# Kernel optimization log

Hardware: AMD Instinct MI355X
Metric: run time of the kernel (lower is better)

The kernel has to match this reference:

```python
import jax, jax.numpy as jnp
import numpy as np

# Static config (matches init_kwargs)
DIM = 1024
INTER = 512
E = 8          # n_routed_experts
TOP_K = 2      # n_activated_experts
ROUTE_SCALE = 1.0


def setup_inputs() -> dict:
    key = jax.random.key(0)
    ks = jax.random.split(key, 8)
    s_d = 1.0 / np.sqrt(DIM)
    s_f = 1.0 / np.sqrt(INTER)
    x = jax.random.normal(ks[0], (2, 2048, DIM), dtype=jnp.float32)
    gate_w = jax.random.uniform(ks[1], (E, DIM), jnp.float32, -s_d, s_d)
    # routed expert weights, stacked: gate/up are [E, F, D], down is [E, D, F]
    wg = jax.random.uniform(ks[2], (E, INTER, DIM), jnp.float32, -s_d, s_d)
    wu = jax.random.uniform(ks[3], (E, INTER, DIM), jnp.float32, -s_d, s_d)
    wd = jax.random.uniform(ks[4], (E, DIM, INTER), jnp.float32, -s_f, s_f)
    # shared expert (n_shared_experts = 1)
    sg = jax.random.uniform(ks[5], (INTER, DIM), jnp.float32, -s_d, s_d)
    su = jax.random.uniform(ks[6], (INTER, DIM), jnp.float32, -s_d, s_d)
    sd = jax.random.uniform(ks[7], (DIM, INTER), jnp.float32, -s_f, s_f)
    return {"x": x, "gate_w": gate_w, "wg": wg, "wu": wu, "wd": wd,
            "sg": sg, "su": su, "sd": sd}


def reference(x, gate_w, wg, wu, wd, sg, su, sd):
    B, S, D = x.shape
    xf = x.reshape(-1, D)                       # [N, D]
    N = xf.shape[0]

    # ---- Gate (eval mode: no expert_bias, softmax scoring, 1 group) ----
    scores = jax.nn.softmax(xf @ gate_w.T, axis=-1)          # [N, E]
    _, idx = jax.lax.top_k(scores, TOP_K)                    # [N, K]
    weights = jnp.take_along_axis(scores, idx, axis=-1) * ROUTE_SCALE  # [N, K]

    # Combine weights as dense [N, E] (scatter-add of top-k weights) --
    # equivalent to the sort/dispatch + weighted scatter_add combine.
    cw = jnp.zeros((N, E), dtype=xf.dtype)
    cw = cw.at[jnp.arange(N)[:, None], idx].add(weights)     # [N, E]

    # ---- Routed experts: SwiGLU per expert ----
    g = jnp.einsum('nd,efd->nef', xf, wg)                    # [N, E, F]
    u = jnp.einsum('nd,efd->nef', xf, wu)                    # [N, E, F]
    h = jax.nn.silu(g) * u                                   # [N, E, F]
    y = jnp.einsum('nef,edf->ned', h, wd)                    # [N, E, D]
    routed = jnp.einsum('ned,ne->nd', y, cw)                 # [N, D]

    # ---- Shared expert (always active) ----
    shared = (jax.nn.silu(xf @ sg.T) * (xf @ su.T)) @ sd.T   # [N, D]

    return (routed + shared).reshape(B, S, D)
```

## Files before the change

### kernel.cpp

```cpp
#include <hip/hip_runtime.h>
#include <hip/hip_bf16.h>

constexpr int NTOK = 4096;
constexpr int DIMD = 1024;
constexpr int FINT = 512;
constexpr int NEXP = 8;

typedef __attribute__((ext_vector_type(8))) short bf16x8;
typedef __attribute__((ext_vector_type(4))) float f32x4;
typedef __attribute__((ext_vector_type(8))) unsigned short u16x8;

__device__ __forceinline__ f32x4 mfma16(bf16x8 a, bf16x8 b, f32x4 c) {
  return __builtin_amdgcn_mfma_f32_16x16x32_bf16(a, b, c, 0, 0, 0);
}

__device__ __forceinline__ void gload16(const void* g, void* l) {
  __builtin_amdgcn_global_load_lds(
      (const __attribute__((address_space(1))) void*)g,
      (__attribute__((address_space(3))) void*)l, 16, 0, 0);
}

__device__ __forceinline__ unsigned short f2bf(float f) {
  unsigned u = __float_as_uint(f);
  u += 0x7fffu + ((u >> 16) & 1u);
  return (unsigned short)(u >> 16);
}

__global__ __launch_bounds__(256) void cast_all(
    const float* __restrict__ x,  const float* __restrict__ wg,
    const float* __restrict__ wu, const float* __restrict__ wd,
    const float* __restrict__ sg, const float* __restrict__ su,
    const float* __restrict__ sd,
    unsigned short* __restrict__ xb,  unsigned short* __restrict__ w1b,
    unsigned short* __restrict__ wdb, unsigned short* __restrict__ s1b,
    unsigned short* __restrict__ sdb) {
  const int seg = blockIdx.y;
  const int i = blockIdx.x * 256 + threadIdx.x;
  const float* src; unsigned short* dst;
  size_t si = (size_t)i * 8, di;
  int n8;
  if (seg == 0) {
    n8 = NTOK * DIMD / 8; if (i >= n8) return;
    src = x; dst = xb; di = si;
  } else if (seg == 1 || seg == 2) {
    n8 = NEXP * FINT * DIMD / 8; if (i >= n8) return;
    int e = (int)(si >> 19), f = (int)((si >> 10) & 511), d = (int)(si & 1023);
    int r = ((f >> 4) << 5) + (seg == 2 ? 16 : 0) + (f & 15);
    src = (seg == 1) ? wg : wu; dst = w1b;
    di = (((size_t)e << 10) + r) * 1024 + d;
  } else if (seg == 3) {
    n8 = NEXP * DIMD * FINT / 8; if (i >= n8) return;
    src = wd; dst = wdb; di = si;
  } else if (seg == 4 || seg == 5) {
    n8 = FINT * DIMD / 8; if (i >= n8) return;
    int f = (int)((si >> 10) & 511), d = (int)(si & 1023);
    int r = ((f >> 4) << 5) + (seg == 5 ? 16 : 0) + (f & 15);
    src = (seg == 4) ? sg : su; dst = s1b;
    di = (size_t)r * 1024 + d;
  } else {
    n8 = DIMD * FINT / 8; if (i >= n8) return;
    src = sd; dst = sdb; di = si;
  }
  const float4* s4 = (const float4*)(src + si);
  float4 a = s4[0], b = s4[1];
  u16x8 o;
  o[0] = f2bf(a.x); o[1] = f2bf(a.y); o[2] = f2bf(a.z); o[3] = f2bf(a.w);
  o[4] = f2bf(b.x); o[5] = f2bf(b.y); o[6] = f2bf(b.z); o[7] = f2bf(b.w);
  *(u16x8*)(dst + di) = o;
}

__global__ __launch_bounds__(256) void gate_logits(const float* __restrict__ x,
                                                   const float* __restrict__ gw,
                                                   int* __restrict__ eid,
                                                   float2* __restrict__ w12) {
  const int wid = threadIdx.x >> 6;
  const int lane = threadIdx.x & 63;
  const int n = blockIdx.x * 4 + wid;

  const float4* xr = (const float4*)(x + (size_t)n * DIMD);
  float4 xv[4];
#pragma unroll
  for (int j = 0; j < 4; ++j) xv[j] = xr[lane + 64 * j];

  double acc[NEXP];
#pragma unroll
  for (int e = 0; e < NEXP; ++e) {
    const float4* g = (const float4*)(gw + (size_t)e * DIMD);
    double a = 0.0;
#pragma unroll
    for (int j = 0; j < 4; ++j) {
      float4 gv = g[lane + 64 * j];
      a += (double)xv[j].x * (double)gv.x + (double)xv[j].y * (double)gv.y
         + (double)xv[j].z * (double)gv.z + (double)xv[j].w * (double)gv.w;
    }
    acc[e] = a;
  }
#pragma unroll
  for (int e = 0; e < NEXP; ++e) {
#pragma unroll
    for (int off = 32; off > 0; off >>= 1) acc[e] += __shfl_xor(acc[e], off);
  }

  if (lane == 0) {
    float logit[NEXP];
#pragma unroll
    for (int e = 0; e < NEXP; ++e) logit[e] = (float)acc[e];
    int i1 = 0; float v1 = logit[0];
#pragma unroll
    for (int e = 1; e < NEXP; ++e) if (logit[e] > v1) { v1 = logit[e]; i1 = e; }
    int i2 = -1; float v2 = -1e30f;
#pragma unroll
    for (int e = 0; e < NEXP; ++e) if (e != i1 && logit[e] > v2) { v2 = logit[e]; i2 = e; }
    float s = 0.f;
#pragma unroll
    for (int e = 0; e < NEXP; ++e) s += expf(logit[e] - v1);
    float w1 = 1.f / s;
    float w2 = expf(v2 - v1) / s;
    eid[n] = i1 | (i2 << 4);
    w12[n] = make_float2(w1, w2);
  }
}

__global__ __launch_bounds__(1024) void dispatch_scan(const int* __restrict__ eid,
                                                      const float2* __restrict__ w12,
                                                      int* __restrict__ cnt,
                                                      int* __restrict__ rowTok,
                                                      float* __restrict__ rowW,
                                                      int2* __restrict__ gslot) {
  const int th = threadIdx.x;
  const int lane = th & 63;
  const int wv = th >> 6;

  int e0[4], e1[4];
  float2 wp[4];
  unsigned long long c0 = 0, c1 = 0;
#pragma unroll
  for (int j = 0; j < 4; ++j) {
    int n = th * 4 + j;
    int p = eid[n];
    wp[j] = w12[n];
    int a = p & 15, b = (p >> 4) & 15;
    e0[j] = a; e1[j] = b;
    unsigned long long ia = 1ull << (16 * (a & 3));
    if (a < 4) c0 += ia; else c1 += ia;
    unsigned long long ib = 1ull << (16 * (b & 3));
    if (b < 4) c0 += ib; else c1 += ib;
  }

  unsigned long long s0 = c0, s1 = c1;
#pragma unroll
  for (int off = 1; off < 64; off <<= 1) {
    unsigned long long u0 = __shfl_up(s0, off);
    unsigned long long u1 = __shfl_up(s1, off);
    if (lane >= off) { s0 += u0; s1 += u1; }
  }

  __shared__ unsigned long long wt0[16], wt1[16];
  __shared__ int ebaseS[NEXP];
  if (lane == 63) { wt0[wv] = s0; wt1[wv] = s1; }
  __syncthreads();

  unsigned long long b0 = 0, b1 = 0;
  for (int w2 = 0; w2 < 16; ++w2)
    if (w2 < wv) { b0 += wt0[w2]; b1 += wt1[w2]; }

  if (th == 0) {
    unsigned long long t0 = 0, t1 = 0;
    for (int w2 = 0; w2 < 16; ++w2) { t0 += wt0[w2]; t1 += wt1[w2]; }
    int tot[NEXP];
#pragma unroll
    for (int e = 0; e < 4; ++e) {
      tot[e]     = (int)((t0 >> (16 * e)) & 0xffff);
      tot[e + 4] = (int)((t1 >> (16 * e)) & 0xffff);
    }
    int run = 0;
#pragma unroll
    for (int e = 0; e < NEXP; ++e) {
      cnt[e] = tot[e];
      cnt[8 + e] = run;
      ebaseS[e] = run;
      run += tot[e];
    }
  }

  unsigned long long x0 = b0 + s0 - c0;
  unsigned long long x1 = b1 + s1 - c1;

  __shared__ unsigned short posL[1024][8];
#pragma unroll
  for (int e = 0; e < 4; ++e) {
    posL[th][e]     = (unsigned short)((x0 >> (16 * e)) & 0xffff);
    posL[th][e + 4] = (unsigned short)((x1 >> (16 * e)) & 0xffff);
  }
  __syncthreads();

#pragma unroll
  for (int j = 0; j < 4; ++j) {
    int n = th * 4 + j;
    int a = e0[j];
    int pa = posL[th][a]; posL[th][a] = (unsigned short)(pa + 1);
    rowTok[a * NTOK + pa] = n; rowW[a * NTOK + pa] = wp[j].x;
    int b = e1[j];
    int pb = posL[th][b]; posL[th][b] = (unsigned short)(pb + 1);
    rowTok[b * NTOK + pb] = n; rowW[b * NTOK + pb] = wp[j].y;
    gslot[n] = make_int2(ebaseS[a] + pa, ebaseS[b] + pb);
  }
}


__global__ __launch_bounds__(512, 1) void gemm1_fused(
    const unsigned short* __restrict__ xb,
    const unsigned short* __restrict__ w1b,
    const unsigned short* __restrict__ s1b,
    unsigned short* __restrict__ hb,
    unsigned short* __restrict__ hs,
    const int* __restrict__ cnt,
    const int* __restrict__ rowTok,
    const unsigned short* __restrict__ zpg) {
  extern __shared__ unsigned char L[];
  const int e = blockIdx.x >> 2, ty = blockIdx.x & 3;
  const int tx = blockIdx.y;
  const bool RT = (e < NEXP);
  const int Te = RT ? cnt[e] : NTOK;
  const int m0 = tx * 256;
  if (m0 >= Te) return;
  const int n0 = ty * 256;

  const int t = threadIdx.x;
  const int w = t >> 6, lane = t & 63;
  const int wr = w >> 2, wc = w & 3;
  const int fr = lane & 15, hi = lane >> 4;
  const int koffl = ((hi ^ ((fr >> 1) & 3)) << 4);

  const unsigned short* w1e = RT ? w1b + (size_t)e * DIMD * DIMD : s1b;

  const unsigned short* apD[2];
  const unsigned short* bpD[2];
  int aoff[2], boff[2];
#pragma unroll
  for (int j = 0; j < 2; ++j) {
    int c = w * 128 + j * 64 + lane;
    int rowL = c >> 2;
    int seff = (c & 3) ^ ((c >> 3) & 3);
    int grow = m0 + rowL;
    const unsigned short* p;
    if (RT) p = (grow < Te) ? xb + (size_t)rowTok[e * NTOK + grow] * DIMD : zpg;
    else    p = xb + (size_t)grow * DIMD;
    apD[j] = p + seff * 8;
    bpD[j] = w1e + (size_t)(n0 + rowL) * DIMD + seff * 8;
    aoff[j] = c * 16;
    boff[j] = 65536 + c * 16;
  }

  f32x4 acc[8][4];
  f32x4 zero = {0.f, 0.f, 0.f, 0.f};
#pragma unroll
  for (int m = 0; m < 8; ++m)
#pragma unroll
    for (int n = 0; n < 4; ++n) acc[m][n] = zero;

  auto STAGE = [&](int buf, int tt, int q) {
    int slab = (buf * 2 + q) * 16384;
#pragma unroll
    for (int j = 0; j < 2; ++j) {
      gload16(apD[j] + tt * 64 + q * 32, L + slab + aoff[j]);
      gload16(bpD[j] + tt * 64 + q * 32, L + slab + boff[j]);
    }
  };
  auto COMPUTE = [&](int buf, int q) {
    int slab = (buf * 2 + q) * 16384;
    const unsigned char* LA = L + slab;
    const unsigned char* LB = L + 65536 + slab;
    bf16x8 Af[8], Bf[4];
#pragma unroll
    for (int m = 0; m < 8; ++m)
      Af[m] = *(const bf16x8*)(LA + (wr * 128 + m * 16 + fr) * 64 + koffl);
#pragma unroll
    for (int n = 0; n < 4; ++n)
      Bf[n] = *(const bf16x8*)(LB + (wc * 64 + n * 16 + fr) * 64 + koffl);
    __builtin_amdgcn_s_setprio(1);
#pragma unroll
    for (int n = 0; n < 4; ++n)
#pragma unroll
      for (int m = 0; m < 8; ++m) acc[m][n] = mfma16(Af[m], Bf[n], acc[m][n]);
    __builtin_amdgcn_s_setprio(0);
  };

  asm volatile("s_waitcnt vmcnt(0)" ::: "memory");
  __builtin_amdgcn_sched_barrier(0);
  STAGE(0, 0, 0);
  STAGE(0, 0, 1);

  constexpr int NT = DIMD / 64;
  for (int tt = 0; tt < NT; ++tt) {
    int buf = tt & 1;
#pragma unroll
    for (int q = 0; q < 2; ++q) {
      if (tt < NT - 1 || q == 0) asm volatile("s_waitcnt vmcnt(4)" ::: "memory");
      else                       asm volatile("s_waitcnt vmcnt(0)" ::: "memory");
      __builtin_amdgcn_sched_barrier(0);
      __builtin_amdgcn_s_barrier();
      __builtin_amdgcn_sched_barrier(0);
      if (tt + 1 < NT) STAGE(buf ^ 1, tt + 1, q);
      COMPUTE(buf, q);
    }
  }

  unsigned short* hbase = RT ? hb + (size_t)cnt[8 + e] * FINT : hs;
  const int fbase = ty * 128 + wc * 32 + fr;
#pragma unroll
  for (int m = 0; m < 8; ++m) {
#pragma unroll
    for (int r = 0; r < 4; ++r) {
      int row = m0 + wr * 128 + m * 16 + hi * 4 + r;
      if (row < Te) {
        float g0 = acc[m][0][r], u0 = acc[m][1][r];
        float g1 = acc[m][2][r], u1 = acc[m][3][r];
        hbase[(size_t)row * FINT + fbase]      = f2bf(g0 / (1.f + expf(-g0)) * u0);
        hbase[(size_t)row * FINT + fbase + 16] = f2bf(g1 / (1.f + expf(-g1)) * u1);
      }
    }
  }
}

__global__ __launch_bounds__(512, 1) void gemm2_fused(
    const unsigned short* __restrict__ hb,
    const unsigned short* __restrict__ hs,
    const unsigned short* __restrict__ wdb,
    const unsigned short* __restrict__ sdb,
    float* __restrict__ ybuf,
    float* __restrict__ out,
    const int* __restrict__ cnt,
    const float* __restrict__ rowW,
    const unsigned short* __restrict__ zpg) {
  extern __shared__ unsigned char L[];
  const int e = blockIdx.x >> 2, ty = blockIdx.x & 3;
  const int tx = blockIdx.y;
  const bool RT = (e < NEXP);
  const int Te = RT ? cnt[e] : NTOK;
  const int m0 = tx * 256;
  if (m0 >= Te) return;
  const int n0 = ty * 256;

  const int t = threadIdx.x;
  const int w = t >> 6, lane = t & 63;
  const int wr = w >> 2, wc = w & 3;
  const int fr = lane & 15, hi = lane >> 4;
  const int koffl = ((hi ^ ((fr >> 1) & 3)) << 4);

  const int gbase = RT ? cnt[8 + e] : 0;
  const unsigned short* he  = RT ? hb + (size_t)gbase * FINT : hs;
  const unsigned short* wde = RT ? wdb + (size_t)e * DIMD * FINT : sdb;

  const unsigned short* apD[2];
  const unsigned short* bpD[2];
  int aoff[2], boff[2];
#pragma unroll
  for (int j = 0; j < 2; ++j) {
    int c = w * 128 + j * 64 + lane;
    int rowL = c >> 2;
    int seff = (c & 3) ^ ((c >> 3) & 3);
    int grow = m0 + rowL;
    apD[j] = ((grow < Te) ? he + (size_t)grow * FINT : zpg) + seff * 8;
    bpD[j] = wde + (size_t)(n0 + rowL) * FINT + seff * 8;
    aoff[j] = c * 16;
    boff[j] = 65536 + c * 16;
  }

  f32x4 acc[8][4];
  f32x4 zero = {0.f, 0.f, 0.f, 0.f};
#pragma unroll
  for (int m = 0; m < 8; ++m)
#pragma unroll
    for (int n = 0; n < 4; ++n) acc[m][n] = zero;

  auto STAGE = [&](int buf, int tt, int q) {
    int slab = (buf * 2 + q) * 16384;
#pragma unroll
    for (int j = 0; j < 2; ++j) {
      gload16(apD[j] + tt * 64 + q * 32, L + slab + aoff[j]);
      gload16(bpD[j] + tt * 64 + q * 32, L + slab + boff[j]);
    }
  };
  auto COMPUTE = [&](int buf, int q) {
    int slab = (buf * 2 + q) * 16384;
    const unsigned char* LA = L + slab;
    const unsigned char* LB = L + 65536 + slab;
    bf16x8 Af[8], Bf[4];
#pragma unroll
    for (int m = 0; m < 8; ++m)
      Af[m] = *(const bf16x8*)(LA + (wr * 128 + m * 16 + fr) * 64 + koffl);
#pragma unroll
    for (int n = 0; n < 4; ++n)
      Bf[n] = *(const bf16x8*)(LB + (wc * 64 + n * 16 + fr) * 64 + koffl);
    __builtin_amdgcn_s_setprio(1);
#pragma unroll
    for (int n = 0; n < 4; ++n)
#pragma unroll
      for (int m = 0; m < 8; ++m) acc[m][n] = mfma16(Af[m], Bf[n], acc[m][n]);
    __builtin_amdgcn_s_setprio(0);
  };

  asm volatile("s_waitcnt vmcnt(0)" ::: "memory");
  __builtin_amdgcn_sched_barrier(0);
  STAGE(0, 0, 0);
  STAGE(0, 0, 1);

  constexpr int NT = FINT / 64;
  for (int tt = 0; tt < NT; ++tt) {
    int buf = tt & 1;
#pragma unroll
    for (int q = 0; q < 2; ++q) {
      if (tt < NT - 1 || q == 0) asm volatile("s_waitcnt vmcnt(4)" ::: "memory");
      else                       asm volatile("s_waitcnt vmcnt(0)" ::: "memory");
      __builtin_amdgcn_sched_barrier(0);
      __builtin_amdgcn_s_barrier();
      __builtin_amdgcn_sched_barrier(0);
      if (tt + 1 < NT) STAGE(buf ^ 1, tt + 1, q);
      COMPUTE(buf, q);
    }
  }

  const int colb = n0 + wc * 64;
#pragma unroll
  for (int m = 0; m < 8; ++m) {
#pragma unroll
    for (int r = 0; r < 4; ++r) {
      int row = m0 + wr * 128 + m * 16 + hi * 4 + r;
      if (row < Te) {
        if (RT) {
          float wt = rowW[e * NTOK + row];
          float* yr = ybuf + (size_t)(gbase + row) * DIMD;
#pragma unroll
          for (int n = 0; n < 4; ++n)
            yr[colb + n * 16 + fr] = wt * acc[m][n][r];
        } else {
          float* orow = out + (size_t)row * DIMD;
#pragma unroll
          for (int n = 0; n < 4; ++n)
            orow[colb + n * 16 + fr] = acc[m][n][r];
        }
      }
    }
  }
}

__global__ __launch_bounds__(256) void combine(const float* __restrict__ ybuf,
                                               const int2* __restrict__ gslot,
                                               float* __restrict__ out) {
  const int n = blockIdx.x;
  const int t = threadIdx.x;
  int2 gs = gslot[n];
  const float4* y1 = (const float4*)(ybuf + (size_t)gs.x * DIMD);
  const float4* y2 = (const float4*)(ybuf + (size_t)gs.y * DIMD);
  float4* o = (float4*)(out + (size_t)n * DIMD);
  float4 a = o[t], b = y1[t], c = y2[t];
  a.x += b.x + c.x; a.y += b.y + c.y; a.z += b.z + c.z; a.w += b.w + c.w;
  o[t] = a;
}

extern "C" void kernel_launch(void* const* d_in, const int* in_sizes, int n_in,
                              void* d_out, int out_size, void* d_ws, size_t ws_size,
                              hipStream_t stream) {
  const float* x  = (const float*)d_in[0];
  const float* gw = (const float*)d_in[1];
  const float* wg = (const float*)d_in[2];
  const float* wu = (const float*)d_in[3];
  const float* wd = (const float*)d_in[4];
  const float* sg = (const float*)d_in[5];
  const float* su = (const float*)d_in[6];
  const float* sd = (const float*)d_in[7];
  float* out = (float*)d_out;

  char* ws = (char*)d_ws;
  size_t off = 0;
  auto alloc = [&](size_t bytes) -> char* {
    char* p = ws + off;
    off += (bytes + 255) & ~(size_t)255;
    return p;
  };
  unsigned short* xb  = (unsigned short*)alloc((size_t)NTOK * DIMD * 2);
  unsigned short* w1b = (unsigned short*)alloc((size_t)NEXP * DIMD * DIMD * 2);
  unsigned short* wdb = (unsigned short*)alloc((size_t)NEXP * DIMD * FINT * 2);
  unsigned short* s1b = (unsigned short*)alloc((size_t)DIMD * DIMD * 2);
  unsigned short* sdb = (unsigned short*)alloc((size_t)DIMD * FINT * 2);
  unsigned short* hb  = (unsigned short*)alloc((size_t)2 * NTOK * FINT * 2);
  unsigned short* hs  = (unsigned short*)alloc((size_t)NTOK * FINT * 2);
  float*         ybuf = (float*)alloc((size_t)2 * NTOK * DIMD * 4);
  int*            cnt = (int*)alloc(256);
  int*         rowTok = (int*)alloc((size_t)NEXP * NTOK * 4);
  float*         rowW = (float*)alloc((size_t)NEXP * NTOK * 4);
  unsigned short* zpg = (unsigned short*)alloc((size_t)DIMD * 2);
  int*            eid = (int*)alloc((size_t)NTOK * 4);
  float2*         w12 = (float2*)alloc((size_t)NTOK * 8);
  int2*         gslot = (int2*)alloc((size_t)NTOK * 8);
  if (off > ws_size) return;

  hipFuncSetAttribute((const void*)gemm1_fused,
                      hipFuncAttributeMaxDynamicSharedMemorySize, 131072);
  hipFuncSetAttribute((const void*)gemm2_fused,
                      hipFuncAttributeMaxDynamicSharedMemorySize, 131072);

  hipMemsetAsync(zpg, 0, (size_t)DIMD * 2, stream);

  cast_all<<<dim3(2048, 7), 256, 0, stream>>>(x, wg, wu, wd, sg, su, sd,
                                              xb, w1b, wdb, s1b, sdb);

  gate_logits<<<NTOK / 4, 256, 0, stream>>>(x, gw, eid, w12);
  dispatch_scan<<<1, 1024, 0, stream>>>(eid, w12, cnt, rowTok, rowW, gslot);

  gemm1_fused<<<dim3(36, 16), 512, 131072, stream>>>(xb, w1b, s1b, hb, hs,
                                                     cnt, rowTok, zpg);
  gemm2_fused<<<dim3(36, 16), 512, 131072, stream>>>(hb, hs, wdb, sdb, ybuf, out,
                                                     cnt, rowW, zpg);
  combine<<<NTOK, 256, 0, stream>>>(ybuf, gslot, out);
}
```

Baseline: 114.5 us.

## Fold gate into cast kernel and restructure GEMM K-loop to one barrier pair per tile

```diff
diff --git a/kernel.cpp b/kernel.cpp
--- a/kernel.cpp
+++ b/kernel.cpp
@@ -30,11 +30,64 @@
     const float* __restrict__ x,  const float* __restrict__ wg,
     const float* __restrict__ wu, const float* __restrict__ wd,
     const float* __restrict__ sg, const float* __restrict__ su,
-    const float* __restrict__ sd,
+    const float* __restrict__ sd, const float* __restrict__ gw,
     unsigned short* __restrict__ xb,  unsigned short* __restrict__ w1b,
     unsigned short* __restrict__ wdb, unsigned short* __restrict__ s1b,
-    unsigned short* __restrict__ sdb) {
+    unsigned short* __restrict__ sdb,
+    int* __restrict__ eid, float2* __restrict__ w12) {
   const int seg = blockIdx.y;
+
+  if (seg == 7) {
+    if (blockIdx.x >= NTOK / 4) return;
+    const int wid = threadIdx.x >> 6;
+    const int lane = threadIdx.x & 63;
+    const int n = blockIdx.x * 4 + wid;
+
+    const float4* xr = (const float4*)(x + (size_t)n * DIMD);
+    float4 xv[4];
+#pragma unroll
+    for (int j = 0; j < 4; ++j) xv[j] = xr[lane + 64 * j];
+
+    double acc[NEXP];
+#pragma unroll
+    for (int e = 0; e < NEXP; ++e) {
+      const float4* g = (const float4*)(gw + (size_t)e * DIMD);
+      double a = 0.0;
+#pragma unroll
+      for (int j = 0; j < 4; ++j) {
+        float4 gv = g[lane + 64 * j];
+        a += (double)xv[j].x * (double)gv.x + (double)xv[j].y * (double)gv.y
+           + (double)xv[j].z * (double)gv.z + (double)xv[j].w * (double)gv.w;
+      }
+      acc[e] = a;
+    }
+#pragma unroll
+    for (int e = 0; e < NEXP; ++e) {
+#pragma unroll
+      for (int off = 32; off > 0; off >>= 1) acc[e] += __shfl_xor(acc[e], off);
+    }
+
+    if (lane == 0) {
+      float logit[NEXP];
+#pragma unroll
+      for (int e = 0; e < NEXP; ++e) logit[e] = (float)acc[e];
+      int i1 = 0; float v1 = logit[0];
+#pragma unroll
+      for (int e = 1; e < NEXP; ++e) if (logit[e] > v1) { v1 = logit[e]; i1 = e; }
+      int i2 = -1; float v2 = -1e30f;
+#pragma unroll
+      for (int e = 0; e < NEXP; ++e) if (e != i1 && logit[e] > v2) { v2 = logit[e]; i2 = e; }
+      float s = 0.f;
+#pragma unroll
+      for (int e = 0; e < NEXP; ++e) s += expf(logit[e] - v1);
+      float w1 = 1.f / s;
+      float w2 = expf(v2 - v1) / s;
+      eid[n] = i1 | (i2 << 4);
+      w12[n] = make_float2(w1, w2);
+    }
+    return;
+  }
+
   const int i = blockIdx.x * 256 + threadIdx.x;
   const float* src; unsigned short* dst;
   size_t si = (size_t)i * 8, di;
@@ -69,58 +122,6 @@
   *(u16x8*)(dst + di) = o;
 }
 
-__global__ __launch_bounds__(256) void gate_logits(const float* __restrict__ x,
-                                                   const float* __restrict__ gw,
-                                                   int* __restrict__ eid,
-                                                   float2* __restrict__ w12) {
-  const int wid = threadIdx.x >> 6;
-  const int lane = threadIdx.x & 63;
-  const int n = blockIdx.x * 4 + wid;
-
-  const float4* xr = (const float4*)(x + (size_t)n * DIMD);
-  float4 xv[4];
-#pragma unroll
-  for (int j = 0; j < 4; ++j) xv[j] = xr[lane + 64 * j];
-
-  double acc[NEXP];
-#pragma unroll
-  for (int e = 0; e < NEXP; ++e) {
-    const float4* g = (const float4*)(gw + (size_t)e * DIMD);
-    double a = 0.0;
-#pragma unroll
-    for (int j = 0; j < 4; ++j) {
-      float4 gv = g[lane + 64 * j];
-      a += (double)xv[j].x * (double)gv.x + (double)xv[j].y * (double)gv.y
-         + (double)xv[j].z * (double)gv.z + (double)xv[j].w * (double)gv.w;
-    }
-    acc[e] = a;
-  }
-#pragma unroll
-  for (int e = 0; e < NEXP; ++e) {
-#pragma unroll
-    for (int off = 32; off > 0; off >>= 1) acc[e] += __shfl_xor(acc[e], off);
-  }
-
-  if (lane == 0) {
-    float logit[NEXP];
-#pragma unroll
-    for (int e = 0; e < NEXP; ++e) logit[e] = (float)acc[e];
-    int i1 = 0; float v1 = logit[0];
-#pragma unroll
-    for (int e = 1; e < NEXP; ++e) if (logit[e] > v1) { v1 = logit[e]; i1 = e; }
-    int i2 = -1; float v2 = -1e30f;
-#pragma unroll
-    for (int e = 0; e < NEXP; ++e) if (e != i1 && logit[e] > v2) { v2 = logit[e]; i2 = e; }
-    float s = 0.f;
-#pragma unroll
-    for (int e = 0; e < NEXP; ++e) s += expf(logit[e] - v1);
-    float w1 = 1.f / s;
-    float w2 = expf(v2 - v1) / s;
-    eid[n] = i1 | (i2 << 4);
-    w12[n] = make_float2(w1, w2);
-  }
-}
-
 __global__ __launch_bounds__(1024) void dispatch_scan(const int* __restrict__ eid,
                                                       const float2* __restrict__ w12,
                                                       int* __restrict__ cnt,
@@ -267,43 +268,46 @@
       gload16(bpD[j] + tt * 64 + q * 32, L + slab + boff[j]);
     }
   };
-  auto COMPUTE = [&](int buf, int q) {
-    int slab = (buf * 2 + q) * 16384;
-    const unsigned char* LA = L + slab;
-    const unsigned char* LB = L + 65536 + slab;
-    bf16x8 Af[8], Bf[4];
-#pragma unroll
-    for (int m = 0; m < 8; ++m)
-      Af[m] = *(const bf16x8*)(LA + (wr * 128 + m * 16 + fr) * 64 + koffl);
-#pragma unroll
-    for (int n = 0; n < 4; ++n)
-      Bf[n] = *(const bf16x8*)(LB + (wc * 64 + n * 16 + fr) * 64 + koffl);
+  auto TILE = [&](int buf) {
+    bf16x8 Af[2][8], Bf[2][4];
+#pragma unroll
+    for (int q = 0; q < 2; ++q) {
+      int slab = (buf * 2 + q) * 16384;
+      const unsigned char* LA = L + slab;
+      const unsigned char* LB = L + 65536 + slab;
+#pragma unroll
+      for (int m = 0; m < 8; ++m)
+        Af[q][m] = *(const bf16x8*)(LA + (wr * 128 + m * 16 + fr) * 64 + koffl);
+#pragma unroll
+      for (int n = 0; n < 4; ++n)
+        Bf[q][n] = *(const bf16x8*)(LB + (wc * 64 + n * 16 + fr) * 64 + koffl);
+    }
     __builtin_amdgcn_s_setprio(1);
 #pragma unroll
-    for (int n = 0; n < 4; ++n)
-#pragma unroll
-      for (int m = 0; m < 8; ++m) acc[m][n] = mfma16(Af[m], Bf[n], acc[m][n]);
+    for (int q = 0; q < 2; ++q)
+#pragma unroll
+      for (int n = 0; n < 4; ++n)
+#pragma unroll
+        for (int m = 0; m < 8; ++m)
+          acc[m][n] = mfma16(Af[q][m], Bf[q][n], acc[m][n]);
     __builtin_amdgcn_s_setprio(0);
   };
 
-  asm volatile("s_waitcnt vmcnt(0)" ::: "memory");
-  __builtin_amdgcn_sched_barrier(0);
   STAGE(0, 0, 0);
   STAGE(0, 0, 1);
 
   constexpr int NT = DIMD / 64;
   for (int tt = 0; tt < NT; ++tt) {
     int buf = tt & 1;
-#pragma unroll
-    for (int q = 0; q < 2; ++q) {
-      if (tt < NT - 1 || q == 0) asm volatile("s_waitcnt vmcnt(4)" ::: "memory");
-      else                       asm volatile("s_waitcnt vmcnt(0)" ::: "memory");
-      __builtin_amdgcn_sched_barrier(0);
-      __builtin_amdgcn_s_barrier();
-      __builtin_amdgcn_sched_barrier(0);
-      if (tt + 1 < NT) STAGE(buf ^ 1, tt + 1, q);
-      COMPUTE(buf, q);
-    }
+    if (tt + 1 < NT) { STAGE(buf ^ 1, tt + 1, 0); STAGE(buf ^ 1, tt + 1, 1); }
+    if (tt + 1 < NT) asm volatile("s_waitcnt vmcnt(8)" ::: "memory");
+    else             asm volatile("s_waitcnt vmcnt(0)" ::: "memory");
+    __builtin_amdgcn_sched_barrier(0);
+    __builtin_amdgcn_s_barrier();
+    __builtin_amdgcn_sched_barrier(0);
+    TILE(buf);
+    __builtin_amdgcn_sched_barrier(0);
+    __builtin_amdgcn_s_barrier();
   }
 
   unsigned short* hbase = RT ? hb + (size_t)cnt[8 + e] * FINT : hs;
@@ -382,43 +386,46 @@
       gload16(bpD[j] + tt * 64 + q * 32, L + slab + boff[j]);
     }
   };
-  auto COMPUTE = [&](int buf, int q) {
-    int slab = (buf * 2 + q) * 16384;
-    const unsigned char* LA = L + slab;
-    const unsigned char* LB = L + 65536 + slab;
-    bf16x8 Af[8], Bf[4];
-#pragma unroll
-    for (int m = 0; m < 8; ++m)
-      Af[m] = *(const bf16x8*)(LA + (wr * 128 + m * 16 + fr) * 64 + koffl);
-#pragma unroll
-    for (int n = 0; n < 4; ++n)
-      Bf[n] = *(const bf16x8*)(LB + (wc * 64 + n * 16 + fr) * 64 + koffl);
+  auto TILE = [&](int buf) {
+    bf16x8 Af[2][8], Bf[2][4];
+#pragma unroll
+    for (int q = 0; q < 2; ++q) {
+      int slab = (buf * 2 + q) * 16384;
+      const unsigned char* LA = L + slab;
+      const unsigned char* LB = L + 65536 + slab;
+#pragma unroll
+      for (int m = 0; m < 8; ++m)
+        Af[q][m] = *(const bf16x8*)(LA + (wr * 128 + m * 16 + fr) * 64 + koffl);
+#pragma unroll
+      for (int n = 0; n < 4; ++n)
+        Bf[q][n] = *(const bf16x8*)(LB + (wc * 64 + n * 16 + fr) * 64 + koffl);
+    }
     __builtin_amdgcn_s_setprio(1);
 #pragma unroll
-    for (int n = 0; n < 4; ++n)
-#pragma unroll
-      for (int m = 0; m < 8; ++m) acc[m][n] = mfma16(Af[m], Bf[n], acc[m][n]);
+    for (int q = 0; q < 2; ++q)
+#pragma unroll
+      for (int n = 0; n < 4; ++n)
+#pragma unroll
+        for (int m = 0; m < 8; ++m)
+          acc[m][n] = mfma16(Af[q][m], Bf[q][n], acc[m][n]);
     __builtin_amdgcn_s_setprio(0);
   };
 
-  asm volatile("s_waitcnt vmcnt(0)" ::: "memory");
-  __builtin_amdgcn_sched_barrier(0);
   STAGE(0, 0, 0);
   STAGE(0, 0, 1);
 
   constexpr int NT = FINT / 64;
   for (int tt = 0; tt < NT; ++tt) {
     int buf = tt & 1;
-#pragma unroll
-    for (int q = 0; q < 2; ++q) {
-      if (tt < NT - 1 || q == 0) asm volatile("s_waitcnt vmcnt(4)" ::: "memory");
-      else                       asm volatile("s_waitcnt vmcnt(0)" ::: "memory");
-      __builtin_amdgcn_sched_barrier(0);
-      __builtin_amdgcn_s_barrier();
-      __builtin_amdgcn_sched_barrier(0);
-      if (tt + 1 < NT) STAGE(buf ^ 1, tt + 1, q);
-      COMPUTE(buf, q);
-    }
+    if (tt + 1 < NT) { STAGE(buf ^ 1, tt + 1, 0); STAGE(buf ^ 1, tt + 1, 1); }
+    if (tt + 1 < NT) asm volatile("s_waitcnt vmcnt(8)" ::: "memory");
+    else             asm volatile("s_waitcnt vmcnt(0)" ::: "memory");
+    __builtin_amdgcn_sched_barrier(0);
+    __builtin_amdgcn_s_barrier();
+    __builtin_amdgcn_sched_barrier(0);
+    TILE(buf);
+    __builtin_amdgcn_sched_barrier(0);
+    __builtin_amdgcn_s_barrier();
   }
 
   const int colb = n0 + wc * 64;
@@ -503,10 +510,9 @@
 
   hipMemsetAsync(zpg, 0, (size_t)DIMD * 2, stream);
 
-  cast_all<<<dim3(2048, 7), 256, 0, stream>>>(x, wg, wu, wd, sg, su, sd,
-                                              xb, w1b, wdb, s1b, sdb);
-
-  gate_logits<<<NTOK / 4, 256, 0, stream>>>(x, gw, eid, w12);
+  cast_all<<<dim3(2048, 8), 256, 0, stream>>>(x, wg, wu, wd, sg, su, sd, gw,
+                                              xb, w1b, wdb, s1b, sdb, eid, w12);
+
   dispatch_scan<<<1, 1024, 0, stream>>>(eid, w12, cnt, rowTok, rowW, gslot);
 
   gemm1_fused<<<dim3(36, 16), 512, 131072, stream>>>(xb, w1b, s1b, hb, hs,
```

Result: slower. 125.7 us (+9.8%).
